# Performance work log

Hardware: AMD Instinct MI355X
Metric: run time of the kernel (lower is better)

## Reference

```python
import jax, jax.numpy as jnp
import numpy as np

NUM_HEADS = 16
D_MODEL = 1024
D_K = D_MODEL // NUM_HEADS


def setup_inputs() -> dict:
    key = jax.random.key(0)
    ks = jax.random.split(key, 11)
    B, S, D = 1, 4096, D_MODEL
    scale = 1.0 / np.sqrt(D)
    return {
        "Q": jax.random.normal(ks[0], (B, S, D), jnp.float32),
        "K": jax.random.normal(ks[1], (B, S, D), jnp.float32),
        "V": jax.random.normal(ks[2], (B, S, D), jnp.float32),
        "W_Q": jax.random.normal(ks[3], (D, D), jnp.float32) * scale,
        "b_Q": jax.random.normal(ks[4], (D,), jnp.float32) * 0.02,
        "W_K": jax.random.normal(ks[5], (D, D), jnp.float32) * scale,
        "b_K": jax.random.normal(ks[6], (D,), jnp.float32) * 0.02,
        "W_V": jax.random.normal(ks[7], (D, D), jnp.float32) * scale,
        "b_V": jax.random.normal(ks[8], (D,), jnp.float32) * 0.02,
        "W_O": jax.random.normal(ks[9], (D, D), jnp.float32) * scale,
        "b_O": jax.random.normal(ks[10], (D,), jnp.float32) * 0.02,
    }


def _split_heads(x):
    # (B, S, D) -> (B, H, S, d_k)
    B, S, _ = x.shape
    return x.reshape(B, S, NUM_HEADS, D_K).transpose(0, 2, 1, 3)


def reference(Q, K, V, W_Q, b_Q, W_K, b_K, W_V, b_V, W_O, b_O):
    q = _split_heads(Q @ W_Q + b_Q)  # (B, H, S, d_k)
    k = _split_heads(K @ W_K + b_K)
    v = _split_heads(V @ W_V + b_V)
    inv_sqrt_dk = jnp.asarray(1.0 / np.sqrt(D_K), q.dtype)
    scores = jnp.einsum("bhqd,bhkd->bhqk", q, k) * inv_sqrt_dk  # (B, H, S, S)
    weights = jax.nn.softmax(scores, axis=-1)
    out = jnp.einsum("bhqk,bhkd->bhqd", weights, v)  # (B, H, S, d_k)
    B, _, S, _ = out.shape
    combined = out.transpose(0, 2, 1, 3).reshape(B, S, D_MODEL)
    return combined @ W_O + b_O
```

## Files before the change

kernel.cpp:

```cpp
#include <hip/hip_runtime.h>

typedef float f32x4 __attribute__((ext_vector_type(4)));
typedef float f32x16 __attribute__((ext_vector_type(16)));
typedef short bf16x8 __attribute__((ext_vector_type(8)));
typedef unsigned u32x2 __attribute__((ext_vector_type(2)));
typedef unsigned short u16;

#define S_LEN 4096
#define DMODEL 1024
#define NH 16
#define DK 64

#define SCALE_Q 0.18033688f

static __device__ __forceinline__ u16 f2bf(float x) {
  union { float f; unsigned u; } v; v.f = x;
  unsigned r = v.u + 0x7fffu + ((v.u >> 16) & 1u);
  return (u16)(r >> 16);
}

#if __has_builtin(__builtin_amdgcn_exp2f)
#define EXP2F __builtin_amdgcn_exp2f
#else
#define EXP2F exp2f
#endif

static __device__ __forceinline__ unsigned pkbf(float lo, float hi) {
  unsigned r;
  asm("v_cvt_pk_bf16_f32 %0, %1, %2" : "=v"(r) : "v"(lo), "v"(hi));
  return r;
}

static __device__ __forceinline__ void plswap(unsigned& a, unsigned& b, int hi) {
#if __has_builtin(__builtin_amdgcn_permlane32_swap)
  u32x2 r = __builtin_amdgcn_permlane32_swap(a, b, false, false);
  a = r.x; b = r.y;
  (void)hi;
#else
  unsigned ax = __shfl_xor(a, 32), bx = __shfl_xor(b, 32);
  unsigned na = hi ? bx : a;
  unsigned nb = hi ? b : ax;
  a = na; b = nb;
#endif
}

static __device__ __forceinline__ void gload16(const void* g, void* l) {
  void* gg = (void*)g;
  __builtin_amdgcn_global_load_lds(
      (__attribute__((address_space(1))) void*)gg,
      (__attribute__((address_space(3))) void*)l, 16, 0, 0);
}

__global__ __launch_bounds__(256) void wcast_t(const float* __restrict__ W,
                                               u16* __restrict__ Wt) {
  __shared__ float t[32][33];
  const int x = threadIdx.x, y = threadIdx.y;
  const int n0 = blockIdx.x * 32, k0 = blockIdx.y * 32;
#pragma unroll
  for (int i = 0; i < 4; ++i)
    t[y + 8 * i][x] = W[(size_t)(k0 + y + 8 * i) * DMODEL + n0 + x];
  __syncthreads();
#pragma unroll
  for (int i = 0; i < 4; ++i)
    Wt[(size_t)(n0 + y + 8 * i) * DMODEL + k0 + x] = f2bf(t[x][y + 8 * i]);
}

__global__ __launch_bounds__(256) void castbf(const float* __restrict__ in,
                                              u16* __restrict__ out, int n8) {
  int i = blockIdx.x * 256 + threadIdx.x;
  const int stride = gridDim.x * 256;
  for (; i < n8; i += stride) {
    float4 a = ((const float4*)in)[2 * i];
    float4 b = ((const float4*)in)[2 * i + 1];
    union { ushort4 u[2]; int4 q; } t;
    t.u[0].x = f2bf(a.x); t.u[0].y = f2bf(a.y);
    t.u[0].z = f2bf(a.z); t.u[0].w = f2bf(a.w);
    t.u[1].x = f2bf(b.x); t.u[1].y = f2bf(b.y);
    t.u[1].z = f2bf(b.z); t.u[1].w = f2bf(b.w);
    ((int4*)out)[i] = t.q;
  }
}

template <int MODE>
__global__ __launch_bounds__(256) void pgemm(const u16* __restrict__ Abase,
                                             const u16* __restrict__ Btbase,
                                             const float* __restrict__ bq,
                                             const float* __restrict__ bk,
                                             const float* __restrict__ bv,
                                             void* __restrict__ outbase) {
  __shared__ __align__(16) char Al[8192];
  __shared__ __align__(16) char Bl[16384];
  const int nblk = gridDim.x, cpx = nblk >> 3;
  const int b0 = blockIdx.x;
  const int bid = (b0 & 7) * cpx + (b0 >> 3);
  const int z = bid >> 9;
  const int rem = bid & 511;
  const int nb = rem & 7, mb = rem >> 3;
  const int m0 = mb * 64, n0 = nb * 128;
  const int tid = threadIdx.x, lane = tid & 63, wid = tid >> 6;
  const int gq = lane >> 4, c16 = lane & 15;
  const int wm2 = (wid >> 1) * 32, wn2 = (wid & 1) * 64;
  const char* Ab = (const char*)(Abase + (size_t)z * S_LEN * DMODEL);
  const char* Bb = (const char*)(Btbase + (size_t)z * DMODEL * DMODEL);
  const float* bias = (z == 0) ? bq : (z == 1 ? bk : bv);
  const float scale = (MODE == 0 && z == 0) ? SCALE_Q : 1.0f;

  f32x4 acc[2][4] = {};

  for (int kt = 0; kt < 16; ++kt) {
    const int kb = kt * 128;
#pragma unroll
    for (int p = 0; p < 2; ++p) {
      int lin = p * 4096 + tid * 16;
      int row = lin >> 7;
      int colg = (lin & 127) ^ ((row & 7) << 4);
      gload16(Ab + (size_t)(m0 + row) * 2048 + kb + colg,
              Al + p * 4096 + wid * 1024);
    }
#pragma unroll
    for (int p = 0; p < 4; ++p) {
      int lin = p * 4096 + tid * 16;
      int row = lin >> 7;
      int colg = (lin & 127) ^ ((row & 7) << 4);
      gload16(Bb + (size_t)(n0 + row) * 2048 + kb + colg,
              Bl + p * 4096 + wid * 1024);
    }
    __syncthreads();
#pragma unroll
    for (int kk = 0; kk < 2; ++kk) {
      bf16x8 a[2], b[4];
#pragma unroll
      for (int m = 0; m < 2; ++m) {
        int row = wm2 + m * 16 + c16;
        a[m] = *(const bf16x8*)(Al + row * 128 +
                                ((kk * 64 + gq * 16) ^ ((row & 7) << 4)));
      }
#pragma unroll
      for (int n = 0; n < 4; ++n) {
        int row = wn2 + n * 16 + c16;
        b[n] = *(const bf16x8*)(Bl + row * 128 +
                                ((kk * 64 + gq * 16) ^ ((row & 7) << 4)));
      }
#pragma unroll
      for (int m = 0; m < 2; ++m)
#pragma unroll
        for (int n = 0; n < 4; ++n)
          acc[m][n] =
              __builtin_amdgcn_mfma_f32_16x16x32_bf16(a[m], b[n], acc[m][n], 0, 0, 0);
    }
    __syncthreads();
  }

#pragma unroll
  for (int m = 0; m < 2; ++m) {
#pragma unroll
    for (int n = 0; n < 4; ++n) {
      const int row = m0 + wm2 + m * 16 + gq * 4;
      const int col = n0 + wn2 + n * 16 + c16;
      const float bb = bias[col];
      if (MODE == 1) {
        float* of = (float*)outbase;
#pragma unroll
        for (int j = 0; j < 4; ++j)
          of[(size_t)(row + j) * DMODEL + col] = acc[m][n][j] + bb;
      } else if (z == 2) {
        u16* ov = (u16*)outbase + (size_t)2 * S_LEN * DMODEL;
        ushort4 u;
        u.x = f2bf(acc[m][n][0] + bb);
        u.y = f2bf(acc[m][n][1] + bb);
        u.z = f2bf(acc[m][n][2] + bb);
        u.w = f2bf(acc[m][n][3] + bb);
        *(ushort4*)(ov + ((size_t)(col >> 6) * DK + (col & 63)) * S_LEN + row) = u;
      } else {
        u16* oq = (u16*)outbase + (size_t)z * S_LEN * DMODEL;
#pragma unroll
        for (int j = 0; j < 4; ++j)
          oq[((size_t)(col >> 6) * S_LEN + row + j) * DK + (col & 63)] =
              f2bf((acc[m][n][j] + bb) * scale);
      }
    }
  }
}

__global__ __launch_bounds__(256) void attn2(const u16* __restrict__ q,
                                             const u16* __restrict__ k,
                                             const u16* __restrict__ vt,
                                             float* __restrict__ Opart,
                                             float* __restrict__ Lpart) {
  __shared__ __align__(16) char smem[32768];
  const int bid0 = blockIdx.x;
  const int bid = (bid0 & 7) * 128 + (bid0 >> 3);
  const int h = bid >> 6;
  const int kvh = (bid >> 5) & 1;
  const int qblk = bid & 31;
  const int tid = threadIdx.x;
  const int wid = tid >> 6, lane = tid & 63;
  const int l31 = lane & 31, hi = lane >> 5;

  const char* kpb = (const char*)k + (size_t)h * S_LEN * (DK * 2);
  const char* vtb = (const char*)vt + (size_t)h * DK * (S_LEN * 2);

  const int q0w = qblk * 128 + wid * 32;
  const u16* qrow = q + ((size_t)h * S_LEN + q0w + l31) * DK;
  bf16x8 qf[4];
#pragma unroll
  for (int dt = 0; dt < 4; ++dt)
    qf[dt] = *(const bf16x8*)(qrow + dt * 16 + hi * 8);

  f32x16 o0 = {}, o1 = {};
  float lacc = 0.f;

  const int woff = wid << 10;
  const int kt0 = kvh * (S_LEN / 128);
  const int kt1 = kt0 + (S_LEN / 128);

  const int swz = (l31 & 7) << 4;
  int dsa[4];
#pragma unroll
  for (int dt = 0; dt < 4; ++dt)
    dsa[dt] = (l31 << 7) + ((dt * 32 + hi * 16) ^ swz);

  const int lin0 = tid * 16, lin1 = 4096 + tid * 16;
  const int sw0 = lin0 ^ (((lin0 >> 7) & 7) << 4);
  const int sw1 = lin1 ^ (((lin1 >> 7) & 7) << 4);
  const char* gk0 = kpb + (size_t)kt0 * 8192 + sw0;
  const char* gk1 = kpb + (size_t)kt0 * 8192 + sw1;
  const char* gv0 = vtb + (size_t)(lin0 >> 7) * 8192 + (size_t)kt0 * 128 + (sw0 & 127);
  const char* gv1 = vtb + (size_t)(lin1 >> 7) * 8192 + (size_t)kt0 * 128 + (sw1 & 127);

  gload16(gk0, smem + woff);          gk0 += 8192;
  gload16(gk1, smem + 4096 + woff);   gk1 += 8192;
  gload16(gv0, smem + 8192 + woff);   gv0 += 128;
  gload16(gv1, smem + 12288 + woff);  gv1 += 128;
  __syncthreads();

  auto body = [&](const int CUR, const int NXT, bool doStage) {
    if (doStage) {
      gload16(gk0, smem + NXT + woff);          gk0 += 8192;
      gload16(gk1, smem + NXT + 4096 + woff);   gk1 += 8192;
      gload16(gv0, smem + NXT + 8192 + woff);   gv0 += 128;
      gload16(gv1, smem + NXT + 12288 + woff);  gv1 += 128;
    }
    const char* kb = smem + CUR;
    const char* vb = smem + CUR + 8192;

    f32x16 st0 = {}, st1 = {};
    __builtin_amdgcn_s_setprio(1);
#pragma unroll
    for (int dt = 0; dt < 4; ++dt) {
      bf16x8 k0 = *(const bf16x8*)(kb + dsa[dt]);
      bf16x8 k1 = *(const bf16x8*)(kb + 4096 + dsa[dt]);
      st0 = __builtin_amdgcn_mfma_f32_32x32x16_bf16(k0, qf[dt], st0, 0, 0, 0);
      st1 = __builtin_amdgcn_mfma_f32_32x32x16_bf16(k1, qf[dt], st1, 0, 0, 0);
    }
    __builtin_amdgcn_s_setprio(0);

    float p0[16], p1[16];
    float s0 = 0.f, s1 = 0.f;
#pragma unroll
    for (int i = 0; i < 16; ++i) { p0[i] = EXP2F(st0[i]); s0 += p0[i]; }
#pragma unroll
    for (int i = 0; i < 16; ++i) { p1[i] = EXP2F(st1[i]); s1 += p1[i]; }
    lacc += s0 + s1;

    union UF { unsigned w[4]; bf16x8 v; };
    UF f[4];
    {
      unsigned a, b;
      a = pkbf(p0[0], p0[1]);   b = pkbf(p0[4], p0[5]);   plswap(a, b, hi);
      f[0].w[0] = a; f[0].w[2] = b;
      a = pkbf(p0[2], p0[3]);   b = pkbf(p0[6], p0[7]);   plswap(a, b, hi);
      f[0].w[1] = a; f[0].w[3] = b;
      a = pkbf(p0[8], p0[9]);   b = pkbf(p0[12], p0[13]); plswap(a, b, hi);
      f[1].w[0] = a; f[1].w[2] = b;
      a = pkbf(p0[10], p0[11]); b = pkbf(p0[14], p0[15]); plswap(a, b, hi);
      f[1].w[1] = a; f[1].w[3] = b;
      a = pkbf(p1[0], p1[1]);   b = pkbf(p1[4], p1[5]);   plswap(a, b, hi);
      f[2].w[0] = a; f[2].w[2] = b;
      a = pkbf(p1[2], p1[3]);   b = pkbf(p1[6], p1[7]);   plswap(a, b, hi);
      f[2].w[1] = a; f[2].w[3] = b;
      a = pkbf(p1[8], p1[9]);   b = pkbf(p1[12], p1[13]); plswap(a, b, hi);
      f[3].w[0] = a; f[3].w[2] = b;
      a = pkbf(p1[10], p1[11]); b = pkbf(p1[14], p1[15]); plswap(a, b, hi);
      f[3].w[1] = a; f[3].w[3] = b;
    }

    __builtin_amdgcn_s_setprio(1);
#pragma unroll
    for (int kt2 = 0; kt2 < 4; ++kt2) {
      bf16x8 v0 = *(const bf16x8*)(vb + dsa[kt2]);
      bf16x8 v1 = *(const bf16x8*)(vb + 4096 + dsa[kt2]);
      o0 = __builtin_amdgcn_mfma_f32_32x32x16_bf16(v0, f[kt2].v, o0, 0, 0, 0);
      o1 = __builtin_amdgcn_mfma_f32_32x32x16_bf16(v1, f[kt2].v, o1, 0, 0, 0);
    }
    __builtin_amdgcn_s_setprio(0);

    __syncthreads();
  };

  for (int kt = kt0; kt < kt1; kt += 2) {
    body(0, 16384, kt + 1 < kt1);
    body(16384, 0, kt + 2 < kt1);
  }

  const float lrow = lacc + __shfl_xor(lacc, 32);
  float* Ob = Opart + ((((size_t)kvh * NH + h) * S_LEN) + q0w + l31) * DK;
#pragma unroll
  for (int g = 0; g < 4; ++g) {
    float4 v0, v1;
    v0.x = o0[g * 4 + 0]; v0.y = o0[g * 4 + 1];
    v0.z = o0[g * 4 + 2]; v0.w = o0[g * 4 + 3];
    *(float4*)(Ob + 8 * g + 4 * hi) = v0;
    v1.x = o1[g * 4 + 0]; v1.y = o1[g * 4 + 1];
    v1.z = o1[g * 4 + 2]; v1.w = o1[g * 4 + 3];
    *(float4*)(Ob + 32 + 8 * g + 4 * hi) = v1;
  }
  Lpart[((size_t)kvh * NH + h) * S_LEN + q0w + l31] = lrow;
}

__global__ __launch_bounds__(256) void combine(const float* __restrict__ Op,
                                               const float* __restrict__ Lp,
                                               u16* __restrict__ comb) {
  const int id = blockIdx.x * 256 + threadIdx.x;
  const int h = id >> 16;
  const int rem = id & 65535;
  const int qv = rem >> 4;
  const int d4 = (rem & 15) << 2;
  const size_t halfO = (size_t)NH * S_LEN * DK;
  const size_t base0 = (((size_t)h * S_LEN) + qv) * DK + d4;
  float4 a = *(const float4*)(Op + base0);
  float4 b = *(const float4*)(Op + halfO + base0);
  float l = Lp[(size_t)h * S_LEN + qv] +
            Lp[(size_t)NH * S_LEN + (size_t)h * S_LEN + qv];
  float inv = 1.f / l;
  ushort4 u;
  u.x = f2bf((a.x + b.x) * inv);
  u.y = f2bf((a.y + b.y) * inv);
  u.z = f2bf((a.z + b.z) * inv);
  u.w = f2bf((a.w + b.w) * inv);
  *(ushort4*)(comb + (size_t)qv * DMODEL + h * DK + d4) = u;
}

extern "C" void kernel_launch(void* const* d_in, const int* in_sizes, int n_in,
                              void* d_out, int out_size, void* d_ws, size_t ws_size,
                              hipStream_t stream) {
  (void)in_sizes; (void)n_in; (void)out_size; (void)ws_size;
  const float* Q   = (const float*)d_in[0];
  const float* K   = (const float*)d_in[1];
  const float* V   = (const float*)d_in[2];
  const float* W_Q = (const float*)d_in[3];
  const float* b_Q = (const float*)d_in[4];
  const float* W_K = (const float*)d_in[5];
  const float* b_K = (const float*)d_in[6];
  const float* W_V = (const float*)d_in[7];
  const float* b_V = (const float*)d_in[8];
  const float* W_O = (const float*)d_in[9];
  const float* b_O = (const float*)d_in[10];
  float* out = (float*)d_out;

  char* ws = (char*)d_ws;
  const size_t MB = 1024 * 1024;
  u16* WtQ = (u16*)ws;
  char* X = ws + 8 * MB;
  u16* Qbf = (u16*)X;
  float* Opart = (float*)X;
  float* Lpart = Opart + (size_t)2 * NH * S_LEN * DK;
  u16* qp   = (u16*)(ws + (size_t)(8 * MB) + 33 * MB);
  u16* kp   = qp + (size_t)S_LEN * DMODEL;
  u16* vtp  = kp + (size_t)S_LEN * DMODEL;
  u16* comb = vtp + (size_t)S_LEN * DMODEL;

  dim3 tb(32, 8);
  dim3 tg(32, 32);
  wcast_t<<<tg, tb, 0, stream>>>(W_Q, WtQ);
  wcast_t<<<tg, tb, 0, stream>>>(W_K, WtQ + (size_t)DMODEL * DMODEL);
  wcast_t<<<tg, tb, 0, stream>>>(W_V, WtQ + (size_t)2 * DMODEL * DMODEL);
  wcast_t<<<tg, tb, 0, stream>>>(W_O, WtQ + (size_t)3 * DMODEL * DMODEL);

  const int n8 = S_LEN * DMODEL / 8;
  castbf<<<2048, 256, 0, stream>>>(Q, Qbf, n8);
  castbf<<<2048, 256, 0, stream>>>(K, Qbf + (size_t)S_LEN * DMODEL, n8);
  castbf<<<2048, 256, 0, stream>>>(V, Qbf + (size_t)2 * S_LEN * DMODEL, n8);

  pgemm<0><<<1536, 256, 0, stream>>>(Qbf, WtQ, b_Q, b_K, b_V, qp);

  attn2<<<1024, 256, 0, stream>>>(qp, kp, vtp, Opart, Lpart);
  combine<<<(NH * S_LEN * DK / 4) / 256, 256, 0, stream>>>(Opart, Lpart, comb);

  pgemm<1><<<512, 256, 0, stream>>>(comb, WtQ + (size_t)3 * DMODEL * DMODEL,
                                    b_O, b_O, b_O, out);
}
```

Measured before the change: 186.2 us.

## Enlarge GEMM tiles, split attention KV four ways, store partials in bf16

The projection GEMM moves from 64x128 to 128x128 block tiles, giving each warp a 64x64 sub-tile for more operand reuse, and the grid shrinks to match. Attention now splits the key range into four chunks instead of two, doubling the block count for parallelism. The partial outputs are written as bf16 rather than fp32, and combine sums four partials. The row-sum accumulation uses paired float2 adds. Together these aim to cut memory traffic and raise occupancy, at the cost of extra bf16 rounding in the partials and more register pressure in the GEMM.

```diff
diff --git a/kernel.cpp b/kernel.cpp
--- a/kernel.cpp
+++ b/kernel.cpp
@@ -1,5 +1,6 @@
 #include <hip/hip_runtime.h>
 
+typedef float f32x2 __attribute__((ext_vector_type(2)));
 typedef float f32x4 __attribute__((ext_vector_type(4)));
 typedef float f32x16 __attribute__((ext_vector_type(16)));
 typedef short bf16x8 __attribute__((ext_vector_type(8)));
@@ -17,6 +18,11 @@
   union { float f; unsigned u; } v; v.f = x;
   unsigned r = v.u + 0x7fffu + ((v.u >> 16) & 1u);
   return (u16)(r >> 16);
+}
+
+static __device__ __forceinline__ float bf2f(u16 x) {
+  union { unsigned u; float f; } v; v.u = ((unsigned)x) << 16;
+  return v.f;
 }
 
 #if __has_builtin(__builtin_amdgcn_exp2f)
@@ -88,29 +94,29 @@
                                              const float* __restrict__ bk,
                                              const float* __restrict__ bv,
                                              void* __restrict__ outbase) {
-  __shared__ __align__(16) char Al[8192];
+  __shared__ __align__(16) char Al[16384];
   __shared__ __align__(16) char Bl[16384];
   const int nblk = gridDim.x, cpx = nblk >> 3;
   const int b0 = blockIdx.x;
   const int bid = (b0 & 7) * cpx + (b0 >> 3);
-  const int z = bid >> 9;
-  const int rem = bid & 511;
+  const int z = (MODE == 0) ? (bid >> 8) : 0;
+  const int rem = bid & 255;
   const int nb = rem & 7, mb = rem >> 3;
-  const int m0 = mb * 64, n0 = nb * 128;
+  const int m0 = mb * 128, n0 = nb * 128;
   const int tid = threadIdx.x, lane = tid & 63, wid = tid >> 6;
   const int gq = lane >> 4, c16 = lane & 15;
-  const int wm2 = (wid >> 1) * 32, wn2 = (wid & 1) * 64;
+  const int wm = (wid >> 1) * 64, wn = (wid & 1) * 64;
   const char* Ab = (const char*)(Abase + (size_t)z * S_LEN * DMODEL);
   const char* Bb = (const char*)(Btbase + (size_t)z * DMODEL * DMODEL);
   const float* bias = (z == 0) ? bq : (z == 1 ? bk : bv);
   const float scale = (MODE == 0 && z == 0) ? SCALE_Q : 1.0f;
 
-  f32x4 acc[2][4] = {};
+  f32x4 acc[4][4] = {};
 
   for (int kt = 0; kt < 16; ++kt) {
     const int kb = kt * 128;
 #pragma unroll
-    for (int p = 0; p < 2; ++p) {
+    for (int p = 0; p < 4; ++p) {
       int lin = p * 4096 + tid * 16;
       int row = lin >> 7;
       int colg = (lin & 127) ^ ((row & 7) << 4);
@@ -128,21 +134,21 @@
     __syncthreads();
 #pragma unroll
     for (int kk = 0; kk < 2; ++kk) {
-      bf16x8 a[2], b[4];
-#pragma unroll
-      for (int m = 0; m < 2; ++m) {
-        int row = wm2 + m * 16 + c16;
+      bf16x8 a[4], b[4];
+#pragma unroll
+      for (int m = 0; m < 4; ++m) {
+        int row = wm + m * 16 + c16;
         a[m] = *(const bf16x8*)(Al + row * 128 +
                                 ((kk * 64 + gq * 16) ^ ((row & 7) << 4)));
       }
 #pragma unroll
       for (int n = 0; n < 4; ++n) {
-        int row = wn2 + n * 16 + c16;
+        int row = wn + n * 16 + c16;
         b[n] = *(const bf16x8*)(Bl + row * 128 +
                                 ((kk * 64 + gq * 16) ^ ((row & 7) << 4)));
       }
 #pragma unroll
-      for (int m = 0; m < 2; ++m)
+      for (int m = 0; m < 4; ++m)
 #pragma unroll
         for (int n = 0; n < 4; ++n)
           acc[m][n] =
@@ -152,11 +158,11 @@
   }
 
 #pragma unroll
-  for (int m = 0; m < 2; ++m) {
+  for (int m = 0; m < 4; ++m) {
 #pragma unroll
     for (int n = 0; n < 4; ++n) {
-      const int row = m0 + wm2 + m * 16 + gq * 4;
-      const int col = n0 + wn2 + n * 16 + c16;
+      const int row = m0 + wm + m * 16 + gq * 4;
+      const int col = n0 + wn + n * 16 + c16;
       const float bb = bias[col];
       if (MODE == 1) {
         float* of = (float*)outbase;
@@ -185,13 +191,13 @@
 __global__ __launch_bounds__(256) void attn2(const u16* __restrict__ q,
                                              const u16* __restrict__ k,
                                              const u16* __restrict__ vt,
-                                             float* __restrict__ Opart,
+                                             u16* __restrict__ Opart,
                                              float* __restrict__ Lpart) {
   __shared__ __align__(16) char smem[32768];
   const int bid0 = blockIdx.x;
-  const int bid = (bid0 & 7) * 128 + (bid0 >> 3);
-  const int h = bid >> 6;
-  const int kvh = (bid >> 5) & 1;
+  const int bid = (bid0 & 7) * 256 + (bid0 >> 3);
+  const int h = bid >> 7;
+  const int kvh = (bid >> 5) & 3;
   const int qblk = bid & 31;
   const int tid = threadIdx.x;
   const int wid = tid >> 6, lane = tid & 63;
@@ -208,11 +214,11 @@
     qf[dt] = *(const bf16x8*)(qrow + dt * 16 + hi * 8);
 
   f32x16 o0 = {}, o1 = {};
-  float lacc = 0.f;
+  f32x2 lacc2 = {0.f, 0.f};
 
   const int woff = wid << 10;
-  const int kt0 = kvh * (S_LEN / 128);
-  const int kt1 = kt0 + (S_LEN / 128);
+  const int kt0 = kvh * 16;
+  const int kt1 = kt0 + 16;
 
   const int swz = (l31 & 7) << 4;
   int dsa[4];
@@ -256,12 +262,16 @@
     __builtin_amdgcn_s_setprio(0);
 
     float p0[16], p1[16];
-    float s0 = 0.f, s1 = 0.f;
-#pragma unroll
-    for (int i = 0; i < 16; ++i) { p0[i] = EXP2F(st0[i]); s0 += p0[i]; }
-#pragma unroll
-    for (int i = 0; i < 16; ++i) { p1[i] = EXP2F(st1[i]); s1 += p1[i]; }
-    lacc += s0 + s1;
+#pragma unroll
+    for (int i = 0; i < 16; ++i) p0[i] = EXP2F(st0[i]);
+#pragma unroll
+    for (int i = 0; i < 16; ++i) p1[i] = EXP2F(st1[i]);
+    f32x2 s2 = {0.f, 0.f};
+#pragma unroll
+    for (int i = 0; i < 8; ++i) { f32x2 t = {p0[2 * i], p0[2 * i + 1]}; s2 += t; }
+#pragma unroll
+    for (int i = 0; i < 8; ++i) { f32x2 t = {p1[2 * i], p1[2 * i + 1]}; s2 += t; }
+    lacc2 += s2;
 
     union UF { unsigned w[4]; bf16x8 v; };
     UF f[4];
@@ -303,22 +313,23 @@
     body(16384, 0, kt + 2 < kt1);
   }
 
+  const float lacc = lacc2.x + lacc2.y;
   const float lrow = lacc + __shfl_xor(lacc, 32);
-  float* Ob = Opart + ((((size_t)kvh * NH + h) * S_LEN) + q0w + l31) * DK;
+  u16* Ob = Opart + ((((size_t)kvh * NH + h) * S_LEN) + q0w + l31) * DK;
 #pragma unroll
   for (int g = 0; g < 4; ++g) {
-    float4 v0, v1;
-    v0.x = o0[g * 4 + 0]; v0.y = o0[g * 4 + 1];
-    v0.z = o0[g * 4 + 2]; v0.w = o0[g * 4 + 3];
-    *(float4*)(Ob + 8 * g + 4 * hi) = v0;
-    v1.x = o1[g * 4 + 0]; v1.y = o1[g * 4 + 1];
-    v1.z = o1[g * 4 + 2]; v1.w = o1[g * 4 + 3];
-    *(float4*)(Ob + 32 + 8 * g + 4 * hi) = v1;
+    ushort4 u0, u1;
+    u0.x = f2bf(o0[g * 4 + 0]); u0.y = f2bf(o0[g * 4 + 1]);
+    u0.z = f2bf(o0[g * 4 + 2]); u0.w = f2bf(o0[g * 4 + 3]);
+    *(ushort4*)(Ob + 8 * g + 4 * hi) = u0;
+    u1.x = f2bf(o1[g * 4 + 0]); u1.y = f2bf(o1[g * 4 + 1]);
+    u1.z = f2bf(o1[g * 4 + 2]); u1.w = f2bf(o1[g * 4 + 3]);
+    *(ushort4*)(Ob + 32 + 8 * g + 4 * hi) = u1;
   }
   Lpart[((size_t)kvh * NH + h) * S_LEN + q0w + l31] = lrow;
 }
 
-__global__ __launch_bounds__(256) void combine(const float* __restrict__ Op,
+__global__ __launch_bounds__(256) void combine(const u16* __restrict__ Op,
                                                const float* __restrict__ Lp,
                                                u16* __restrict__ comb) {
   const int id = blockIdx.x * 256 + threadIdx.x;
@@ -326,18 +337,21 @@
   const int rem = id & 65535;
   const int qv = rem >> 4;
   const int d4 = (rem & 15) << 2;
-  const size_t halfO = (size_t)NH * S_LEN * DK;
-  const size_t base0 = (((size_t)h * S_LEN) + qv) * DK + d4;
-  float4 a = *(const float4*)(Op + base0);
-  float4 b = *(const float4*)(Op + halfO + base0);
-  float l = Lp[(size_t)h * S_LEN + qv] +
-            Lp[(size_t)NH * S_LEN + (size_t)h * S_LEN + qv];
-  float inv = 1.f / l;
+  const size_t str = (size_t)NH * S_LEN * DK;
+  const size_t base = (((size_t)h * S_LEN) + qv) * DK + d4;
+  float o0 = 0.f, o1 = 0.f, o2 = 0.f, o3 = 0.f, l = 0.f;
+#pragma unroll
+  for (int kv = 0; kv < 4; ++kv) {
+    ushort4 u = *(const ushort4*)(Op + kv * str + base);
+    o0 += bf2f(u.x); o1 += bf2f(u.y); o2 += bf2f(u.z); o3 += bf2f(u.w);
+    l += Lp[(size_t)kv * NH * S_LEN + (size_t)h * S_LEN + qv];
+  }
+  const float inv = 1.f / l;
   ushort4 u;
-  u.x = f2bf((a.x + b.x) * inv);
-  u.y = f2bf((a.y + b.y) * inv);
-  u.z = f2bf((a.z + b.z) * inv);
-  u.w = f2bf((a.w + b.w) * inv);
+  u.x = f2bf(o0 * inv);
+  u.y = f2bf(o1 * inv);
+  u.z = f2bf(o2 * inv);
+  u.w = f2bf(o3 * inv);
   *(ushort4*)(comb + (size_t)qv * DMODEL + h * DK + d4) = u;
 }
 
@@ -361,14 +375,13 @@
   char* ws = (char*)d_ws;
   const size_t MB = 1024 * 1024;
   u16* WtQ = (u16*)ws;
-  char* X = ws + 8 * MB;
-  u16* Qbf = (u16*)X;
-  float* Opart = (float*)X;
-  float* Lpart = Opart + (size_t)2 * NH * S_LEN * DK;
-  u16* qp   = (u16*)(ws + (size_t)(8 * MB) + 33 * MB);
+  u16* Qbf = (u16*)(ws + 8 * MB);
+  u16* Opart = (u16*)(ws + 8 * MB);
+  u16* qp   = (u16*)(ws + 40 * MB);
   u16* kp   = qp + (size_t)S_LEN * DMODEL;
   u16* vtp  = kp + (size_t)S_LEN * DMODEL;
   u16* comb = vtp + (size_t)S_LEN * DMODEL;
+  float* Lpart = (float*)(ws + 72 * MB);
 
   dim3 tb(32, 8);
   dim3 tg(32, 32);
@@ -382,11 +395,11 @@
   castbf<<<2048, 256, 0, stream>>>(K, Qbf + (size_t)S_LEN * DMODEL, n8);
   castbf<<<2048, 256, 0, stream>>>(V, Qbf + (size_t)2 * S_LEN * DMODEL, n8);
 
-  pgemm<0><<<1536, 256, 0, stream>>>(Qbf, WtQ, b_Q, b_K, b_V, qp);
-
-  attn2<<<1024, 256, 0, stream>>>(qp, kp, vtp, Opart, Lpart);
-  combine<<<(NH * S_LEN * DK / 4) / 256, 256, 0, stream>>>(Opart, Lpart, comb);
-
-  pgemm<1><<<512, 256, 0, stream>>>(comb, WtQ + (size_t)3 * DMODEL * DMODEL,
+  pgemm<0><<<768, 256, 0, stream>>>(Qbf, WtQ, b_Q, b_K, b_V, qp);
+
+  attn2<<<2048, 256, 0, stream>>>(qp, kp, vtp, Opart, Lpart);
+  combine<<<4096, 256, 0, stream>>>(Opart, Lpart, comb);
+
+  pgemm<1><<<256, 256, 0, stream>>>(comb, WtQ + (size_t)3 * DMODEL * DMODEL,
                                     b_O, b_O, b_O, out);
 }
```

After: 196.0 us. 1.05x slower.
